# Kernel optimization log

Hardware: AMD Instinct MI355X
Metric: run time of the kernel (lower is better)

## Reference

```python
import jax, jax.numpy as jnp
import numpy as np

B, CIN, D, H, W = 2, 64, 64, 64, 64
NUM_CLASSES = 5
STRIDE = 2
NMAX = 32
TOPK = 13
TAL_ALPHA, TAL_BETA = 1.0, 6.0
EPS = 1e-9


def setup_inputs() -> dict:
    key = jax.random.key(0)
    ks = jax.random.split(key, 6)
    features = jax.random.normal(ks[0], (B, CIN, D, H, W), jnp.float32)
    cls_w = jax.random.normal(ks[1], (NUM_CLASSES, CIN, 3, 3, 3), jnp.float32) * 0.02
    cls_b = jnp.zeros((NUM_CLASSES,), jnp.float32)
    off_w = jax.random.normal(ks[2], (3, CIN, 3, 3, 3), jnp.float32) * 0.01
    off_b = jnp.zeros((3,), jnp.float32)
    coords = jax.random.uniform(ks[3], (B, NMAX, 3), jnp.float32, 4.0, float(D * STRIDE) - 4.0)
    cls = jax.random.randint(ks[4], (B, NMAX, 1), 0, NUM_CLASSES).astype(jnp.float32)
    sigma = jax.random.uniform(ks[5], (B, NMAX, 1), jnp.float32, 2.0, 8.0)
    pad = (jnp.arange(NMAX) >= 24)[None, :, None]  # last 8 GT slots are padding
    cls = jnp.where(pad, -100.0, cls)
    labels = jnp.concatenate([coords, cls, sigma], axis=-1)  # B N 5 : x,y,z,class,sigma
    return {"features": features, "cls_w": cls_w, "cls_b": cls_b,
            "off_w": off_w, "off_b": off_b, "labels": labels}


def conv3d(x, w, b):
    y = jax.lax.conv_general_dilated(x, w, (1, 1, 1), 'SAME',
                                     dimension_numbers=('NCDHW', 'OIDHW', 'NCDHW'))
    return y + b[None, :, None, None, None]


def make_anchors():
    g = jnp.stack(jnp.meshgrid(jnp.arange(D), jnp.arange(H), jnp.arange(W), indexing='ij'))
    return (g.astype(jnp.float32) + 0.5) * STRIDE  # (3, D, H, W)


def flatten_bchw(x):
    # B C D H W -> B (D H W) C
    Bsz, C = x.shape[0], x.shape[1]
    return x.transpose(0, 2, 3, 4, 1).reshape(Bsz, -1, C)


def tal_assign(pred_logits, pred_centers, true_labels, true_centers, true_sigmas, valid):
    # pred_logits (B,L,C); pred_centers (B,L,3); true_* (B,N,...); valid (B,N) bool
    Bsz, L, C = pred_logits.shape
    N = true_labels.shape[1]
    d2 = jnp.sum((true_centers[:, :, None, :] - pred_centers[:, None, :, :]) ** 2, -1)  # B N L
    ious = jnp.exp(-d2 / (2.0 * true_sigmas[:, :, None] ** 2))  # keypoint IoU, B N L
    probs = jax.nn.sigmoid(pred_logits).transpose(0, 2, 1)  # B C L
    cls_scores = jnp.take_along_axis(probs, true_labels[:, :, None], axis=1)  # B N L
    align = (cls_scores ** TAL_ALPHA) * (ious ** TAL_BETA)  # alignment metric
    topv, topi = jax.lax.top_k(align, TOPK)
    is_topk = jnp.zeros_like(align).at[
        jnp.arange(Bsz)[:, None, None], jnp.arange(N)[None, :, None], topi
    ].set(jnp.where(topv > EPS, 1.0, 0.0))
    mask_pos = is_topk * valid[:, :, None].astype(align.dtype)  # B N L
    pos_sum = mask_pos.sum(axis=1)  # B L
    # resolve anchors matched to multiple GTs: keep GT with max IoU
    is_max_iou = jax.nn.one_hot(jnp.argmax(ious, axis=1), N, axis=1, dtype=align.dtype)
    mask_pos = jnp.where(pos_sum[:, None, :] > 1, is_max_iou, mask_pos)
    pos_sum = mask_pos.sum(axis=1)
    fg = pos_sum > 0  # B L
    assigned_gt = jnp.argmax(mask_pos, axis=1)  # B L
    assigned_labels = jnp.take_along_axis(true_labels, assigned_gt, axis=1)
    assigned_labels = jnp.where(fg, assigned_labels, C)  # bg_index = C
    assigned_centers = jnp.take_along_axis(true_centers, assigned_gt[:, :, None], axis=1)  # B L 3
    assigned_sigmas = jnp.take_along_axis(true_sigmas, assigned_gt, axis=1)  # B L
    align = align * mask_pos
    max_align = align.max(axis=2, keepdims=True)  # B N 1
    max_iou = (ious * mask_pos).max(axis=2, keepdims=True)
    score = (align * max_iou / (max_align + EPS)).max(axis=1)  # B L
    assigned_scores = jax.nn.one_hot(assigned_labels, C + 1)[..., :C] * score[..., None]  # B L C
    return assigned_labels, assigned_centers, assigned_scores, assigned_sigmas


def detection_loss(logits, offsets, anchors, labels):
    pred_logits = flatten_bchw(logits)               # B L C
    pred_centers = flatten_bchw(anchors + offsets)   # B L 3
    anchor_pts = flatten_bchw(anchors)
    C = pred_logits.shape[-1]
    true_centers = labels[..., :3]
    true_labels_f = labels[..., 3]
    true_sigmas = labels[..., 4]
    valid = true_labels_f != -100.0
    true_labels = jnp.where(valid, true_labels_f, 0.0).astype(jnp.int32)
    assigned = tal_assign(jax.lax.stop_gradient(pred_logits),
                          jax.lax.stop_gradient(pred_centers),
                          true_labels, true_centers, true_sigmas, valid)
    assigned_labels, assigned_centers, assigned_scores, assigned_sigmas = jax.lax.stop_gradient(assigned)
    one_hot_label = jax.nn.one_hot(assigned_labels, C + 1)[..., :C]
    # varifocal loss (alpha=0.75, gamma=2)
    p = jax.nn.sigmoid(pred_logits)
    weight = 0.75 * (p ** 2.0) * (1.0 - one_hot_label) + assigned_scores * one_hot_label
    bce = assigned_scores * jax.nn.softplus(-pred_logits) + (1.0 - assigned_scores) * jax.nn.softplus(pred_logits)
    cls_loss = jnp.sum(weight * bce)
    d = jnp.sum((pred_centers - assigned_centers) ** 2, -1)  # B L
    w = assigned_scores.sum(-1)
    iou = jnp.exp(-d / (2.0 * assigned_sigmas ** 2))
    mask_positive = assigned_labels != C
    reg_loss = jnp.sum(jnp.where(mask_positive, (1.0 - iou) * w, 0.0))
    return (cls_loss + reg_loss) / assigned_scores.sum()


def reference(features, cls_w, cls_b, off_w, off_b, labels):
    logits = conv3d(features, cls_w, cls_b)    # B C D H W
    offsets = conv3d(features, off_w, off_b)   # B 3 D H W
    anchors = jnp.broadcast_to(make_anchors()[None], (features.shape[0], 3, D, H, W))
    loss = detection_loss(logits, offsets, anchors, labels)
    return loss
```

## Files before the change

kernel.cpp:

```cpp
#include <hip/hip_runtime.h>
#include <math.h>

#define NB 2
#define CIN 64
#define DD_ 64
#define HH_ 64
#define WW_ 64
#define NCLS 5
#define LL (DD_*HH_*WW_)
#define NMAXG 32
#define TOPKK 13
#define NSLAB 4

typedef __attribute__((ext_vector_type(8)))  short short8b;
typedef __attribute__((ext_vector_type(16))) float floatx16;

__device__ __forceinline__ float softplusf_(float z){
  return fmaxf(z, 0.f) + log1pf(expf(-fabsf(z)));
}
__device__ __forceinline__ float sigmoidf_(float z){
  return 1.f/(1.f + expf(-z));
}
__device__ __forceinline__ unsigned tobf_u_(float f){
  unsigned u = __float_as_uint(f);
  return (u + 0x7fffu + ((u>>16)&1u)) >> 16;
}
__device__ __forceinline__ short tobf_(float f){
  return (short)tobf_u_(f);
}

__global__ __launch_bounds__(256) void wtrans_kernel(
    const float* __restrict__ cls_w, const float* __restrict__ off_w,
    short* __restrict__ wA, float* __restrict__ bgz)
{
  if (blockIdx.x == 0 && threadIdx.x < 2) bgz[threadIdx.x] = 0.f;
  int idx = blockIdx.x*256 + threadIdx.x;
  if (idx >= 216*64) return;
  int slice = idx >> 6; int lane = idx & 63;
  int cc = slice & 3; int r = slice >> 2;
  int kw = r % 3; int r2 = r / 3;
  int kh = r2 % 3; int rr = r2 / 3;
  int m = lane & 31, khalf = lane >> 5;
  int outch = m & 7;
  int kd = rr - (m >> 3);
  short8b out;
  #pragma unroll
  for (int i=0;i<8;++i){
    int c = cc*16 + khalf*8 + i;
    float wv = 0.f;
    if (kd >= 0 && kd <= 2){
      if (outch < NCLS) wv = cls_w[(outch*CIN + c)*27 + kd*9 + kh*3 + kw];
      else              wv = off_w[((outch-NCLS)*CIN + c)*27 + kd*9 + kh*3 + kw];
    }
    out[i] = tobf_(wv);
  }
  *(short8b*)(wA + (size_t)idx*8) = out;
}

__global__ __launch_bounds__(256) void transpose_kernel(
    const float* __restrict__ feat, short* __restrict__ featT)
{
  const int t = threadIdx.x;
  const int w = t & 63;
  const int hh = t >> 6;
  const int d = blockIdx.x;
  const int h = blockIdx.y*4 + hh;
  const int b = blockIdx.z;
  const float* src = feat + (size_t)b*CIN*LL + (size_t)d*4096 + (size_t)h*64 + w;
  const size_t sp = (size_t)d*4096 + (size_t)h*64 + w;
  #pragma unroll
  for (int cc=0; cc<4; ++cc){
    float f[16];
    #pragma unroll
    for (int j=0;j<16;++j) f[j] = src[(size_t)(cc*16+j)*LL];
    uint4 p0, p1;
    p0.x = (tobf_u_(f[1])<<16)|tobf_u_(f[0]);  p0.y = (tobf_u_(f[3])<<16)|tobf_u_(f[2]);
    p0.z = (tobf_u_(f[5])<<16)|tobf_u_(f[4]);  p0.w = (tobf_u_(f[7])<<16)|tobf_u_(f[6]);
    p1.x = (tobf_u_(f[9])<<16)|tobf_u_(f[8]);  p1.y = (tobf_u_(f[11])<<16)|tobf_u_(f[10]);
    p1.z = (tobf_u_(f[13])<<16)|tobf_u_(f[12]);p1.w = (tobf_u_(f[15])<<16)|tobf_u_(f[14]);
    *(uint4*)(featT + (((size_t)(b*4+cc)*2 + 0)*LL + sp)*8) = p0;
    *(uint4*)(featT + (((size_t)(b*4+cc)*2 + 1)*LL + sp)*8) = p1;
  }
}

__global__ __launch_bounds__(256, 2) void conv_mfma_kernel(
    const short* __restrict__ featT,
    const short* __restrict__ wA,
    const float* __restrict__ cls_b, const float* __restrict__ off_b,
    float* __restrict__ logits_ws,
    float* __restrict__ centers_ws,
    float* __restrict__ bg_sum,
    unsigned* __restrict__ moff_u)
{
  __shared__ short xs[36*132*8];
  __shared__ float bsum[4];

  const int tid = threadIdx.x;
  const int lane = tid & 63, hl = tid >> 6;
  const int col = lane & 31, khalf = lane >> 5;
  const int h0 = blockIdx.x*4, d0 = blockIdx.y*4, b = blockIdx.z;
  const bool edge = (d0==0) || (d0==DD_-4) || (h0==0) || (h0==HH_-4);

  for (int idx = tid; idx < 144; idx += 256){
    int row = idx >> 2, q = idx & 3;
    *(uint4*)(xs + (row*132 + (q>>1)*66 + (q&1)*65)*8) = make_uint4(0,0,0,0);
  }
  if (edge){
    #pragma unroll 1
    for (int row=0; row<36; ++row){
      int d_ = d0-1+row/6, h_ = h0-1+row-6*(row/6);
      if ((unsigned)d_ < 64u && (unsigned)h_ < 64u) continue;
      for (int idx = tid; idx < 128; idx += 256){
        *(uint4*)(xs + (row*132 + (idx>>6)*66 + (idx&63) + 1)*8) = make_uint4(0,0,0,0);
      }
    }
  }

  floatx16 accA = (floatx16)(0.f);
  floatx16 accB = (floatx16)(0.f);

  const short8b* wAv = (const short8b*)wA;

  int vA[3], vB[3];
  #pragma unroll
  for (int kw=0;kw<3;++kw){
    vA[kw] = hl*0 + khalf*528 + (col+kw)*8;
    vB[kw] = vA[kw] + 256;
  }

#define LOADA(dst, ccv, rrv) { \
  _Pragma("unroll") \
  for (int q=0;q<9;++q) dst[q] = wAv[(size_t)((((rrv)*9+q)*4+(ccv)))*64 + lane]; }

#define COMPR(areg, rrv) \
  if ((unsigned)(d0-1+(rrv)) < 64u){ \
    _Pragma("unroll") \
    for (int kh=0;kh<3;++kh){ \
      if ((unsigned)(h0+hl-1+kh) < 64u){ \
        const int rowb = ((rrv)*6 + hl + kh)*1056; \
        _Pragma("unroll") \
        for (int kw=0;kw<3;++kw){ \
          short8b a = areg[kh*3+kw]; \
          short8b b0 = *(const short8b*)(xs + rowb + vA[kw]); \
          accA = __builtin_amdgcn_mfma_f32_32x32x16_bf16(a, b0, accA, 0,0,0); \
          short8b b1 = *(const short8b*)(xs + rowb + vB[kw]); \
          accB = __builtin_amdgcn_mfma_f32_32x32x16_bf16(a, b1, accB, 0,0,0); \
        } } } }

  short8b aP[9], aQ[9];
  LOADA(aP, 0, 0);

  #pragma unroll 1
  for (int cc=0; cc<4; ++cc){
    if (cc) __syncthreads();
    {
      const short* plane = featT + (size_t)(b*4+cc)*2*(size_t)LL*8;
      #pragma unroll
      for (int it=0; it<18; ++it){
        int strip = it*4 + hl;
        int row = strip >> 1, kh2 = strip & 1;
        int d_ = d0 - 1 + row/6, h_ = h0 - 1 + row - 6*(row/6);
        if (!edge || ((unsigned)d_ < 64u && (unsigned)h_ < 64u)){
          const short* src = plane + ((size_t)kh2*LL + (size_t)d_*4096 + (size_t)h_*64 + lane)*8;
          short* dst = xs + (row*132 + kh2*66 + 1)*8;
          __builtin_amdgcn_global_load_lds(
            (const __attribute__((address_space(1))) void*)src,
            (__attribute__((address_space(3))) void*)dst, 16, 0, 0);
        }
      }
    }
    __syncthreads();
    LOADA(aQ, cc, 1);             COMPR(aP, 0);
    LOADA(aP, cc, 2);             COMPR(aQ, 1);
    LOADA(aQ, cc, 3);             COMPR(aP, 2);
    LOADA(aP, cc, 4);             COMPR(aQ, 3);
    LOADA(aQ, cc, 5);             COMPR(aP, 4);
    { int nc = (cc+1)&3; LOADA(aP, nc, 0); }  COMPR(aQ, 5);
  }

  float bg = 0.f, om = 0.f;
  const int h = h0 + hl;
  #pragma unroll
  for (int wh=0; wh<2; ++wh){
    const int w = wh*32 + col;
    #pragma unroll
    for (int dq=0; dq<4; ++dq){
      int d = d0 + dq;
      size_t l = (size_t)d*4096 + (size_t)h*64 + w;
      float v0 = wh ? accB[dq*4+0] : accA[dq*4+0];
      float v1 = wh ? accB[dq*4+1] : accA[dq*4+1];
      float v2 = wh ? accB[dq*4+2] : accA[dq*4+2];
      float v3 = wh ? accB[dq*4+3] : accA[dq*4+3];
      if (khalf == 0){
        float z0 = v0 + cls_b[0]; logits_ws[(size_t)(b*NCLS+0)*LL + l] = z0;
        float z1 = v1 + cls_b[1]; logits_ws[(size_t)(b*NCLS+1)*LL + l] = z1;
        float z2 = v2 + cls_b[2]; logits_ws[(size_t)(b*NCLS+2)*LL + l] = z2;
        float z3 = v3 + cls_b[3]; logits_ws[(size_t)(b*NCLS+3)*LL + l] = z3;
        float p;
        p = sigmoidf_(z0); bg += 0.75f*p*p*softplusf_(z0);
        p = sigmoidf_(z1); bg += 0.75f*p*p*softplusf_(z1);
        p = sigmoidf_(z2); bg += 0.75f*p*p*softplusf_(z2);
        p = sigmoidf_(z3); bg += 0.75f*p*p*softplusf_(z3);
      } else {
        float z4 = v0 + cls_b[4]; logits_ws[(size_t)(b*NCLS+4)*LL + l] = z4;
        float p = sigmoidf_(z4); bg += 0.75f*p*p*softplusf_(z4);
        float o0 = v1 + off_b[0];
        float o1 = v2 + off_b[1];
        float o2 = v3 + off_b[2];
        om = fmaxf(om, fmaxf(fabsf(o0), fmaxf(fabsf(o1), fabsf(o2))));
        float4 ctr;
        ctr.x = ((float)d+0.5f)*2.f + o0;
        ctr.y = ((float)h+0.5f)*2.f + o1;
        ctr.z = ((float)w+0.5f)*2.f + o2;
        ctr.w = 0.f;
        *(float4*)(centers_ws + ((size_t)b*LL + l)*4) = ctr;
      }
    }
  }
  #pragma unroll
  for (int off=32;off;off>>=1){
    bg += __shfl_down(bg, off);
    om = fmaxf(om, __shfl_xor(om, off));
  }
  if (lane == 0){
    bsum[hl] = bg;
    atomicMax(moff_u, __float_as_uint(om));
  }
  __syncthreads();
  if (tid == 0)
    atomicAdd(bg_sum, bsum[0]+bsum[1]+bsum[2]+bsum[3]);
}

__global__ __launch_bounds__(256) void topk_box_kernel(
    const float* __restrict__ logits_ws, const float* __restrict__ centers_ws,
    const float* __restrict__ labels,
    const unsigned* __restrict__ moff_u,
    float* __restrict__ pv, int* __restrict__ pi)
{
  const int bn = blockIdx.x;
  const int slab = blockIdx.y;
  const int b = bn >> 5, n = bn & 31;
  const int tid = threadIdx.x;

  const float* lb = labels + (b*NMAXG + n)*5;
  const float tx = lb[0], ty = lb[1], tz = lb[2];
  const float cf = lb[3];
  const float sg = lb[4];
  const int lab = (cf == -100.f) ? 0 : (int)cf;
  const float m6 = -3.f/(sg*sg);
  const float moff = __uint_as_float(*moff_u);
  const float R = 2.6336f*sg + moff + 0.05f;

  int i0d = (int)ceilf((tx - R - 1.f)*0.5f); if (i0d < 0) i0d = 0;
  int i1d = (int)floorf((tx + R - 1.f)*0.5f); if (i1d > 63) i1d = 63;
  int i0h = (int)ceilf((ty - R - 1.f)*0.5f); if (i0h < 0) i0h = 0;
  int i1h = (int)floorf((ty + R - 1.f)*0.5f); if (i1h > 63) i1h = 63;
  int i0w = (int)ceilf((tz - R - 1.f)*0.5f); if (i0w < 0) i0w = 0;
  int i1w = (int)floorf((tz + R - 1.f)*0.5f); if (i1w > 63) i1w = 63;
  int nd = i1d-i0d+1, nh = i1h-i0h+1, nw = i1w-i0w+1;
  int total = (nd>0 && nh>0 && nw>0) ? nd*nh*nw : 0;
  int lo = (total*slab)/NSLAB, hi = (total*(slab+1))/NSLAB;

  const float* lg = logits_ws + (size_t)(b*NCLS + lab)*LL;
  const float* cb = centers_ws + (size_t)b*LL*4;

  float v[13]; int ix[13];
  #pragma unroll
  for (int j=0;j<13;++j){ v[j]=-1.f; ix[j]=0x7fffffff; }

  for (int idx = lo + tid; idx < hi; idx += 256){
    int r = idx;
    int wi = r % nw; r /= nw;
    int hi2 = r % nh; int di = r / nh;
    int l = (i0d+di)*4096 + (i0h+hi2)*64 + (i0w+wi);
    float4 c4 = *(const float4*)(cb + (size_t)l*4);
    float dx = c4.x-tx, dy = c4.y-ty, dz = c4.z-tz;
    float e = m6*(dx*dx + dy*dy + dz*dz);
    if (e < -20.8f) continue;
    float a = sigmoidf_(lg[l]) * expf(e);
    if (a > v[12]){
      float cv = a; int ci = l;
      #pragma unroll
      for (int j=0;j<13;++j){
        bool take = (cv > v[j]) || (cv == v[j] && ci < ix[j]);
        float nv = take ? cv : v[j];  float ov = take ? v[j] : cv;
        int   ni = take ? ci : ix[j]; int   oi = take ? ix[j] : ci;
        v[j]=nv; ix[j]=ni; cv=ov; ci=oi;
      }
    }
  }

  const int lane = tid & 63, wvi = tid >> 6;
  float mv = -2.f; int mi = 0x7fffffff;
  #pragma unroll 1
  for (int k=0;k<13;++k){
    float bv = v[0]; int bi = ix[0]; int bl = lane;
    #pragma unroll
    for (int off=32; off; off>>=1){
      float ov2 = __shfl_xor(bv, off);
      int oi = __shfl_xor(bi, off);
      int ol = __shfl_xor(bl, off);
      if (ov2 > bv || (ov2 == bv && oi < bi)){ bv=ov2; bi=oi; bl=ol; }
    }
    if (lane == k){ mv = bv; mi = bi; }
    if (lane == bl){
      #pragma unroll
      for (int j=0;j<12;++j){ v[j]=v[j+1]; ix[j]=ix[j+1]; }
      v[12] = -2.f; ix[12] = 0x7fffffff;
    }
  }
  __shared__ float sv2[4*13]; __shared__ int si2[4*13];
  if (lane < 13){ sv2[wvi*13+lane] = mv; si2[wvi*13+lane] = mi; }
  __syncthreads();
  if (wvi == 0){
    float v2 = -2.f; int i2 = 0x7fffffff;
    if (lane < 52){ v2 = sv2[lane]; i2 = si2[lane]; }
    #pragma unroll 1
    for (int k=0;k<13;++k){
      float bv = v2; int bi = i2; int bl = lane;
      #pragma unroll
      for (int off=32; off; off>>=1){
        float ov2 = __shfl_xor(bv, off);
        int oi = __shfl_xor(bi, off);
        int ol = __shfl_xor(bl, off);
        if (ov2 > bv || (ov2 == bv && oi < bi)){ bv=ov2; bi=oi; bl=ol; }
      }
      if (lane == 0){
        pv[(bn*NSLAB+slab)*TOPKK + k] = bv;
        pi[(bn*NSLAB+slab)*TOPKK + k] = bi;
      }
      if (lane == bl) v2 = -2.f;
    }
  }
}

__global__ __launch_bounds__(64) void topk_merge_kernel(
    const float* __restrict__ pv, const int* __restrict__ pi,
    float* __restrict__ tv, int* __restrict__ ti)
{
  const int bn = blockIdx.x;
  const int t = threadIdx.x;
  const int NC = NSLAB*TOPKK;
  float v = -2.f; int ix = 0x7fffffff;
  if (t < NC){ v = pv[bn*NC + t]; ix = pi[bn*NC + t]; }
  #pragma unroll 1
  for (int k=0;k<13;++k){
    float bv = v; int bi = ix; int bl = t;
    #pragma unroll
    for (int off=32; off; off>>=1){
      float ov = __shfl_xor(bv, off);
      int oi = __shfl_xor(bi, off);
      int ol = __shfl_xor(bl, off);
      if (ov > bv || (ov == bv && oi < bi)){ bv=ov; bi=oi; bl=ol; }
    }
    if (t==0){ tv[bn*TOPKK+k]=bv; ti[bn*TOPKK+k]=bi; }
    if (t==bl) v = -2.f;
  }
}

__global__ __launch_bounds__(1024) void finalize_kernel(
    const float* __restrict__ logits_ws, const float* __restrict__ centers_ws,
    const float* __restrict__ labels,
    const float* __restrict__ tv, const int* __restrict__ ti,
    const float* __restrict__ bg_sum, float* __restrict__ out)
{
  const int tid = threadIdx.x;
  __shared__ float gx[64], gy[64], gz[64], gs[64];
  __shared__ int glab[64], gvalid[64];
  __shared__ int hkey[2048], hcnt[2048], hmin[2048];
  __shared__ unsigned maxA[64], maxI[64];
  __shared__ float accD, accC;
  if (tid==0){ accD=0.f; accC=0.f; }
  for (int i=tid;i<2048;i+=1024){ hkey[i]=-1; hcnt[i]=0; hmin[i]=0x7fffffff; }
  if (tid<64){
    const float* lb = labels + tid*5;
    gx[tid]=lb[0]; gy[tid]=lb[1]; gz[tid]=lb[2];
    float cf = lb[3]; gs[tid]=lb[4];
    int val = (cf != -100.f);
    gvalid[tid]=val; glab[tid]= val ? (int)cf : 0;
    maxA[tid]=0u; maxI[tid]=0u;
  }
  __syncthreads();

  const int e = tid;
  bool ok = false; int l = -1; int n = 0; int b = 0;
  if (e < 2*416){
    b = (e >= 416) ? 1 : 0;
    int eb = e - 416*b;
    n = eb/13; int k = eb - 13*n;
    float v = tv[(b*NMAXG+n)*TOPKK + k];
    l = ti[(b*NMAXG+n)*TOPKK + k];
    ok = gvalid[b*32+n] && (v > 1e-9f);
  }
  int slot = -1;
  if (ok){
    unsigned h = (((unsigned)l * 2654435761u) >> 20) & 1023u;
    for (;;){
      int prev = atomicCAS(&hkey[b*1024 + h], -1, l);
      if (prev == -1 || prev == l){ slot = b*1024 + (int)h; break; }
      h = (h+1) & 1023u;
    }
    atomicAdd(&hcnt[slot], 1);
    atomicMin(&hmin[slot], e);
  }
  __syncthreads();

  bool first = ok && (hmin[slot] == e);
  float a=0.f, iou=0.f; int nstar=0;
  if (first){
    float px = centers_ws[((size_t)b*LL + l)*4 + 0];
    float py = centers_ws[((size_t)b*LL + l)*4 + 1];
    float pz = centers_ws[((size_t)b*LL + l)*4 + 2];
    if (hcnt[slot] == 1){
      nstar = n;
    } else {
      float best = -1.f; int bidx = 0;
      #pragma unroll 1
      for (int nn=0;nn<32;++nn){
        float dx=gx[b*32+nn]-px, dy=gy[b*32+nn]-py, dz=gz[b*32+nn]-pz;
        float d2 = dx*dx+dy*dy+dz*dz;
        float io = expf(-d2/(2.f*gs[b*32+nn]*gs[b*32+nn]));
        if (io > best){ best=io; bidx=nn; }
      }
      nstar = bidx;
    }
    int gi = b*32 + nstar;
    float dx=gx[gi]-px, dy=gy[gi]-py, dz=gz[gi]-pz;
    float d2 = dx*dx+dy*dy+dz*dz;
    float sgv = gs[gi];
    iou = expf(-d2/(2.f*sgv*sgv));
    float z = logits_ws[(size_t)(b*NCLS + glab[gi])*LL + l];
    a = sigmoidf_(z) * expf(-3.f*d2/(sgv*sgv));
    atomicMax(&maxA[gi], __float_as_uint(a));
    atomicMax(&maxI[gi], __float_as_uint(iou));
  }
  __syncthreads();

  if (first){
    int gi = b*32 + nstar;
    float mA = __uint_as_float(maxA[gi]);
    float mI = __uint_as_float(maxI[gi]);
    float score = a*mI/(mA + 1e-9f);
    float z = logits_ws[(size_t)(b*NCLS + glab[gi])*LL + l];
    float p = sigmoidf_(z);
    float t2 = log1pf(expf(-fabsf(z)));
    float spz = fmaxf(z,0.f) + t2;
    float spm = fmaxf(-z,0.f) + t2;
    float corr = score*(score*spm + (1.f-score)*spz) - 0.75f*p*p*spz;
    float reg  = (1.f - iou)*score;
    atomicAdd(&accD, score);
    atomicAdd(&accC, corr + reg);
  }
  __syncthreads();
  if (tid==0) out[0] = (bg_sum[0] + accC) / accD;
}

extern "C" void kernel_launch(void* const* d_in, const int* in_sizes, int n_in,
                              void* d_out, int out_size, void* d_ws, size_t ws_size,
                              hipStream_t stream) {
  const float* feat  = (const float*)d_in[0];
  const float* cls_w = (const float*)d_in[1];
  const float* cls_b = (const float*)d_in[2];
  const float* off_w = (const float*)d_in[3];
  const float* off_b = (const float*)d_in[4];
  const float* labels= (const float*)d_in[5];
  float* out = (float*)d_out;

  float* logits_ws  = (float*)d_ws;
  float* centers_ws = logits_ws + (size_t)NB*NCLS*LL;
  float* tv = centers_ws + (size_t)NB*LL*4;
  int*   ti = (int*)(tv + 64*TOPKK);
  float* pv = (float*)(ti + 64*TOPKK);
  int*   pi = (int*)(pv + 64*NSLAB*TOPKK);
  float* bg = (float*)(pi + 64*NSLAB*TOPKK);
  short* wA = (short*)(bg + 16);
  short* featT = wA + 216*64*8;

  wtrans_kernel<<<54, 256, 0, stream>>>(cls_w, off_w, wA, bg);
  transpose_kernel<<<dim3(64,16,2), 256, 0, stream>>>(feat, featT);
  conv_mfma_kernel<<<dim3(16,16,2), 256, 0, stream>>>(
      featT, wA, cls_b, off_b, logits_ws, centers_ws, bg, (unsigned*)(bg+1));
  topk_box_kernel<<<dim3(64,NSLAB), 256, 0, stream>>>(
      logits_ws, centers_ws, labels, (const unsigned*)(bg+1), pv, pi);
  topk_merge_kernel<<<64, 64, 0, stream>>>(pv, pi, tv, ti);
  finalize_kernel<<<1, 1024, 0, stream>>>(
      logits_ws, centers_ws, labels, tv, ti, bg, out);
}
```

Before: 170.5 us.

## Double-buffer LDS feature staging in conv and fuse weight transform into transpose

The conv kernel now keeps two LDS buffers, so the async global-to-LDS load of the next channel chunk is issued before the MFMA work on the current chunk. This is meant to hide load latency behind compute instead of stalling at a barrier on every chunk. LDS use doubles, and launch bounds drop to one block per SM, which lowers occupancy. The weight-transform kernel is also folded into the transpose kernel to save one launch.

```diff
diff --git a/kernel.cpp b/kernel.cpp
--- a/kernel.cpp
+++ b/kernel.cpp
@@ -29,36 +29,10 @@
   return (short)tobf_u_(f);
 }
 
-__global__ __launch_bounds__(256) void wtrans_kernel(
+__global__ __launch_bounds__(256) void transpose_kernel(
+    const float* __restrict__ feat, short* __restrict__ featT,
     const float* __restrict__ cls_w, const float* __restrict__ off_w,
     short* __restrict__ wA, float* __restrict__ bgz)
-{
-  if (blockIdx.x == 0 && threadIdx.x < 2) bgz[threadIdx.x] = 0.f;
-  int idx = blockIdx.x*256 + threadIdx.x;
-  if (idx >= 216*64) return;
-  int slice = idx >> 6; int lane = idx & 63;
-  int cc = slice & 3; int r = slice >> 2;
-  int kw = r % 3; int r2 = r / 3;
-  int kh = r2 % 3; int rr = r2 / 3;
-  int m = lane & 31, khalf = lane >> 5;
-  int outch = m & 7;
-  int kd = rr - (m >> 3);
-  short8b out;
-  #pragma unroll
-  for (int i=0;i<8;++i){
-    int c = cc*16 + khalf*8 + i;
-    float wv = 0.f;
-    if (kd >= 0 && kd <= 2){
-      if (outch < NCLS) wv = cls_w[(outch*CIN + c)*27 + kd*9 + kh*3 + kw];
-      else              wv = off_w[((outch-NCLS)*CIN + c)*27 + kd*9 + kh*3 + kw];
-    }
-    out[i] = tobf_(wv);
-  }
-  *(short8b*)(wA + (size_t)idx*8) = out;
-}
-
-__global__ __launch_bounds__(256) void transpose_kernel(
-    const float* __restrict__ feat, short* __restrict__ featT)
 {
   const int t = threadIdx.x;
   const int w = t & 63;
@@ -81,9 +55,32 @@
     *(uint4*)(featT + (((size_t)(b*4+cc)*2 + 0)*LL + sp)*8) = p0;
     *(uint4*)(featT + (((size_t)(b*4+cc)*2 + 1)*LL + sp)*8) = p1;
   }
-}
-
-__global__ __launch_bounds__(256, 2) void conv_mfma_kernel(
+  if (blockIdx.z == 0 && blockIdx.y == 0 && blockIdx.x < 54){
+    if (blockIdx.x == 0 && t < 2) bgz[t] = 0.f;
+    int idx = blockIdx.x*256 + t;
+    int slice = idx >> 6; int lane = idx & 63;
+    int cc = slice & 3; int r = slice >> 2;
+    int kw = r % 3; int r2 = r / 3;
+    int kh = r2 % 3; int rr = r2 / 3;
+    int m = lane & 31, khalf = lane >> 5;
+    int outch = m & 7;
+    int kd = rr - (m >> 3);
+    short8b out;
+    #pragma unroll
+    for (int i=0;i<8;++i){
+      int c = cc*16 + khalf*8 + i;
+      float wv = 0.f;
+      if (kd >= 0 && kd <= 2){
+        if (outch < NCLS) wv = cls_w[(outch*CIN + c)*27 + kd*9 + kh*3 + kw];
+        else              wv = off_w[((outch-NCLS)*CIN + c)*27 + kd*9 + kh*3 + kw];
+      }
+      out[i] = tobf_(wv);
+    }
+    *(short8b*)(wA + (size_t)idx*8) = out;
+  }
+}
+
+__global__ __launch_bounds__(256, 1) void conv_mfma_kernel(
     const short* __restrict__ featT,
     const short* __restrict__ wA,
     const float* __restrict__ cls_b, const float* __restrict__ off_b,
@@ -92,8 +89,9 @@
     float* __restrict__ bg_sum,
     unsigned* __restrict__ moff_u)
 {
-  __shared__ short xs[36*132*8];
+  __shared__ short xs[2*36*132*8];
   __shared__ float bsum[4];
+  const int BUFS = 36*132*8;
 
   const int tid = threadIdx.x;
   const int lane = tid & 63, hl = tid >> 6;
@@ -101,17 +99,23 @@
   const int h0 = blockIdx.x*4, d0 = blockIdx.y*4, b = blockIdx.z;
   const bool edge = (d0==0) || (d0==DD_-4) || (h0==0) || (h0==HH_-4);
 
-  for (int idx = tid; idx < 144; idx += 256){
-    int row = idx >> 2, q = idx & 3;
-    *(uint4*)(xs + (row*132 + (q>>1)*66 + (q&1)*65)*8) = make_uint4(0,0,0,0);
+  for (int idx = tid; idx < 288; idx += 256){
+    int bufsel = idx / 144;
+    int j = idx - bufsel*144;
+    int row = j >> 2, q = j & 3;
+    *(uint4*)(xs + bufsel*BUFS + (row*132 + (q>>1)*66 + (q&1)*65)*8) = make_uint4(0,0,0,0);
   }
   if (edge){
     #pragma unroll 1
     for (int row=0; row<36; ++row){
       int d_ = d0-1+row/6, h_ = h0-1+row-6*(row/6);
       if ((unsigned)d_ < 64u && (unsigned)h_ < 64u) continue;
-      for (int idx = tid; idx < 128; idx += 256){
-        *(uint4*)(xs + (row*132 + (idx>>6)*66 + (idx&63) + 1)*8) = make_uint4(0,0,0,0);
+      {
+        int idx = tid;
+        int bufsel = idx >> 7;
+        int r = idx & 127;
+        int kh2 = r >> 6, wp = (r & 63) + 1;
+        *(uint4*)(xs + bufsel*BUFS + (row*132 + kh2*66 + wp)*8) = make_uint4(0,0,0,0);
       }
     }
   }
@@ -124,15 +128,32 @@
   int vA[3], vB[3];
   #pragma unroll
   for (int kw=0;kw<3;++kw){
-    vA[kw] = hl*0 + khalf*528 + (col+kw)*8;
+    vA[kw] = khalf*528 + (col+kw)*8;
     vB[kw] = vA[kw] + 256;
   }
+
+#define STAGE(ccv, bufsel) { \
+  const short* plane = featT + (size_t)(b*4+(ccv))*2*(size_t)LL*8; \
+  short* xb_ = xs + (bufsel)*BUFS; \
+  _Pragma("unroll") \
+  for (int it=0; it<18; ++it){ \
+    int strip = it*4 + hl; \
+    int row = strip >> 1, kh2 = strip & 1; \
+    int d_ = d0 - 1 + row/6, h_ = h0 - 1 + row - 6*(row/6); \
+    if (!edge || ((unsigned)d_ < 64u && (unsigned)h_ < 64u)){ \
+      const short* srcp = plane + ((size_t)kh2*LL + (size_t)d_*4096 + (size_t)h_*64 + lane)*8; \
+      short* dstp = xb_ + (row*132 + kh2*66 + 1)*8; \
+      __builtin_amdgcn_global_load_lds( \
+        (const __attribute__((address_space(1))) void*)srcp, \
+        (__attribute__((address_space(3))) void*)dstp, 16, 0, 0); \
+    } \
+  } }
 
 #define LOADA(dst, ccv, rrv) { \
   _Pragma("unroll") \
   for (int q=0;q<9;++q) dst[q] = wAv[(size_t)((((rrv)*9+q)*4+(ccv)))*64 + lane]; }
 
-#define COMPR(areg, rrv) \
+#define COMPR(areg, rrv, xb) \
   if ((unsigned)(d0-1+(rrv)) < 64u){ \
     _Pragma("unroll") \
     for (int kh=0;kh<3;++kh){ \
@@ -141,41 +162,28 @@
         _Pragma("unroll") \
         for (int kw=0;kw<3;++kw){ \
           short8b a = areg[kh*3+kw]; \
-          short8b b0 = *(const short8b*)(xs + rowb + vA[kw]); \
+          short8b b0 = *(const short8b*)((xb) + rowb + vA[kw]); \
           accA = __builtin_amdgcn_mfma_f32_32x32x16_bf16(a, b0, accA, 0,0,0); \
-          short8b b1 = *(const short8b*)(xs + rowb + vB[kw]); \
+          short8b b1 = *(const short8b*)((xb) + rowb + vB[kw]); \
           accB = __builtin_amdgcn_mfma_f32_32x32x16_bf16(a, b1, accB, 0,0,0); \
         } } } }
 
   short8b aP[9], aQ[9];
   LOADA(aP, 0, 0);
+  STAGE(0, 0);
+  __syncthreads();
 
   #pragma unroll 1
   for (int cc=0; cc<4; ++cc){
-    if (cc) __syncthreads();
-    {
-      const short* plane = featT + (size_t)(b*4+cc)*2*(size_t)LL*8;
-      #pragma unroll
-      for (int it=0; it<18; ++it){
-        int strip = it*4 + hl;
-        int row = strip >> 1, kh2 = strip & 1;
-        int d_ = d0 - 1 + row/6, h_ = h0 - 1 + row - 6*(row/6);
-        if (!edge || ((unsigned)d_ < 64u && (unsigned)h_ < 64u)){
-          const short* src = plane + ((size_t)kh2*LL + (size_t)d_*4096 + (size_t)h_*64 + lane)*8;
-          short* dst = xs + (row*132 + kh2*66 + 1)*8;
-          __builtin_amdgcn_global_load_lds(
-            (const __attribute__((address_space(1))) void*)src,
-            (__attribute__((address_space(3))) void*)dst, 16, 0, 0);
-        }
-      }
-    }
-    __syncthreads();
-    LOADA(aQ, cc, 1);             COMPR(aP, 0);
-    LOADA(aP, cc, 2);             COMPR(aQ, 1);
-    LOADA(aQ, cc, 3);             COMPR(aP, 2);
-    LOADA(aP, cc, 4);             COMPR(aQ, 3);
-    LOADA(aQ, cc, 5);             COMPR(aP, 4);
-    { int nc = (cc+1)&3; LOADA(aP, nc, 0); }  COMPR(aQ, 5);
+    const short* xb = xs + (cc&1)*BUFS;
+    if (cc < 3) STAGE(cc+1, (cc+1)&1);
+    LOADA(aQ, cc, 1);             COMPR(aP, 0, xb);
+    LOADA(aP, cc, 2);             COMPR(aQ, 1, xb);
+    LOADA(aQ, cc, 3);             COMPR(aP, 2, xb);
+    LOADA(aP, cc, 4);             COMPR(aQ, 3, xb);
+    LOADA(aQ, cc, 5);             COMPR(aP, 4, xb);
+    { int nc = (cc+1)&3; LOADA(aP, nc, 0); }  COMPR(aQ, 5, xb);
+    if (cc < 3) __syncthreads();
   }
 
   float bg = 0.f, om = 0.f;
@@ -476,8 +484,8 @@
   short* wA = (short*)(bg + 16);
   short* featT = wA + 216*64*8;
 
-  wtrans_kernel<<<54, 256, 0, stream>>>(cls_w, off_w, wA, bg);
-  transpose_kernel<<<dim3(64,16,2), 256, 0, stream>>>(feat, featT);
+  transpose_kernel<<<dim3(64,16,2), 256, 0, stream>>>(
+      feat, featT, cls_w, off_w, wA, bg);
   conv_mfma_kernel<<<dim3(16,16,2), 256, 0, stream>>>(
       featT, wA, cls_b, off_b, logits_ws, centers_ws, bg, (unsigned*)(bg+1));
   topk_box_kernel<<<dim3(64,NSLAB), 256, 0, stream>>>(
```

Measured after the change: 184.3 us. 8.1% more time.
